# Performance work log

Hardware: AMD Instinct MI355X
Metric: run time of the kernel (lower is better)

The kernel has to match this reference:

```python
import jax, jax.numpy as jnp
import numpy as np


def setup_inputs() -> dict:
    key = jax.random.key(0)
    ks = jax.random.split(key, 7)
    B, T, I, H, O = 128, 1024, 300, 128, 64
    s_ih = 1.0 / np.sqrt(H)
    return {
        "x": jax.random.normal(ks[0], (B, T, I), dtype=jnp.float32),
        "W_ih": jax.random.normal(ks[1], (4 * H, I), dtype=jnp.float32) * s_ih,
        "W_hh": jax.random.normal(ks[2], (4 * H, H), dtype=jnp.float32) * s_ih,
        "b_ih": jax.random.normal(ks[3], (4 * H,), dtype=jnp.float32) * s_ih,
        "b_hh": jax.random.normal(ks[4], (4 * H,), dtype=jnp.float32) * s_ih,
        "W1": jax.random.normal(ks[5], (O, H), dtype=jnp.float32) * s_ih,
        "b1": jax.random.normal(ks[6], (O,), dtype=jnp.float32) * s_ih,
    }


def reference(x, W_ih, W_hh, b_ih, b_hh, W1, b1):
    B, T, I = x.shape
    H = W_hh.shape[1]
    # Precompute the input-to-gate projections for all timesteps at once: [B,T,4H]
    x_gates = jnp.einsum("bti,gi->btg", x, W_ih) + b_ih + b_hh

    def step(carry, xg_t):
        h, c = carry
        gates = xg_t + h @ W_hh.T  # [B, 4H]
        i_g, f_g, g_g, o_g = jnp.split(gates, 4, axis=-1)
        i_g = jax.nn.sigmoid(i_g)
        f_g = jax.nn.sigmoid(f_g)
        g_g = jnp.tanh(g_g)
        o_g = jax.nn.sigmoid(o_g)
        c_new = f_g * c + i_g * g_g
        h_new = o_g * jnp.tanh(c_new)
        return (h_new, c_new), h_new

    h0 = jnp.zeros((B, H), dtype=x.dtype)
    c0 = jnp.zeros((B, H), dtype=x.dtype)
    _, all_h = jax.lax.scan(step, (h0, c0), jnp.swapaxes(x_gates, 0, 1))  # [T,B,H]
    h_seq = jnp.swapaxes(all_h, 0, 1)  # [B,T,H]
    # Dropout in eval mode (identity) for a deterministic reference.
    y = jnp.einsum("bth,oh->bto", h_seq, W1) + b1
    return y
```

## Files before the change

### kernel.cpp

```cpp
#include <hip/hip_runtime.h>
#include <hip/hip_fp16.h>

typedef __attribute__((ext_vector_type(8))) short  s16x8;
typedef __attribute__((ext_vector_type(4))) float  f32x4;
typedef __attribute__((ext_vector_type(4))) unsigned short u16x4;
typedef _Float16 f16x2 __attribute__((ext_vector_type(2)));
typedef _Float16 f16x8 __attribute__((ext_vector_type(8)));
typedef unsigned short u16;

#define MFMA16B(A, B, C) __builtin_amdgcn_mfma_f32_16x16x32_bf16((A), (B), (C), 0, 0, 0)
#define MFMA16H(A, B, C) __builtin_amdgcn_mfma_f32_16x16x32_f16((A), (B), (C), 0, 0, 0)

static __device__ __forceinline__ u16 f2bf(float f) {
    union { float f; unsigned u; } v; v.f = f;
    unsigned r = (v.u + 0x7fffu + ((v.u >> 16) & 1u)) >> 16;
    return (u16)r;
}

static __device__ __forceinline__ s16x8 pack_f16x8(float4 a, float4 b) {
    s16x8 r;
    r[0] = (short)__half_as_ushort(__float2half_rn(a.x));
    r[1] = (short)__half_as_ushort(__float2half_rn(a.y));
    r[2] = (short)__half_as_ushort(__float2half_rn(a.z));
    r[3] = (short)__half_as_ushort(__float2half_rn(a.w));
    r[4] = (short)__half_as_ushort(__float2half_rn(b.x));
    r[5] = (short)__half_as_ushort(__float2half_rn(b.y));
    r[6] = (short)__half_as_ushort(__float2half_rn(b.z));
    r[7] = (short)__half_as_ushort(__float2half_rn(b.w));
    return r;
}

static __device__ __forceinline__ unsigned pk2f16(float a, float b) {
    unsigned lo = __half_as_ushort(__float2half_rn(a));
    unsigned hi = __half_as_ushort(__float2half_rn(b));
    return lo | (hi << 16);
}

static __device__ __forceinline__ float hu2f(u16 v) {
    __half_raw hr; hr.x = v; return __half2float(__half(hr));
}

static __device__ __forceinline__ float dot2(unsigned a, unsigned b, float c) {
#if __has_builtin(__builtin_amdgcn_fdot2)
    return __builtin_amdgcn_fdot2(__builtin_bit_cast(f16x2, a),
                                  __builtin_bit_cast(f16x2, b), c, false);
#else
    f16x2 av = __builtin_bit_cast(f16x2, a), bv = __builtin_bit_cast(f16x2, b);
    return fmaf((float)av[0], (float)bv[0], fmaf((float)av[1], (float)bv[1], c));
#endif
}

static __device__ __forceinline__ float sigm(float x) {
    return __builtin_amdgcn_rcpf(1.f + __expf(-x));
}
static __device__ __forceinline__ float tanh_f(float x) {
    float e = __expf(-2.f * x);
    return fmaf(2.f, __builtin_amdgcn_rcpf(1.f + e), -1.f);
}

static __device__ __forceinline__ void wg_barrier() {
    asm volatile("s_waitcnt lgkmcnt(0)\n\ts_barrier" ::: "memory");
}

#define DPPB(v, ctrl) __builtin_bit_cast(float, __builtin_amdgcn_update_dpp(    \
        0, __builtin_bit_cast(int, (v)), (ctrl), 0xf, 0xf, true))

__global__ __launch_bounds__(256, 2)
void k1_gemm_xgates(const float* __restrict__ x, const float* __restrict__ W_ih,
                    const float* __restrict__ b_ih, const float* __restrict__ b_hh,
                    __half* __restrict__ xg) {
    const int n0 = blockIdx.x * 128;
    const int m0 = blockIdx.y * 128;
    const int tid = threadIdx.x;
    const int wave = tid >> 6, lane = tid & 63;
    const int lanelo = lane & 15, quad = lane >> 4;
    const int mw = (wave & 1) * 64, nw = (wave >> 1) * 64;

    __shared__ __align__(16) u16 As[128 * 40];
    __shared__ __align__(16) u16 Bs[128 * 40];

    f32x4 acc[4][4];
#pragma unroll
    for (int i = 0; i < 4; ++i)
#pragma unroll
        for (int j = 0; j < 4; ++j) acc[i][j] = (f32x4)0.f;

    const int srow = tid >> 1;
    const int scol = (tid & 1) * 16;
    const int grow = (srow & 3) * 128 + (n0 >> 2) + (srow >> 2);

    for (int kc = 0; kc < 10; ++kc) {
        const int k0 = kc * 32;
        const float* srcA = x + (size_t)(m0 + srow) * 300 + k0 + scol;
        const float* srcB = W_ih + (size_t)grow * 300 + k0 + scol;
        if (kc < 9) {
#pragma unroll
            for (int i = 0; i < 4; ++i) {
                const int col = scol + i * 4;
                float4 v = *(const float4*)(srcA + i * 4);
                u16x4 w; w.x = f2bf(v.x); w.y = f2bf(v.y); w.z = f2bf(v.z); w.w = f2bf(v.w);
                *(u16x4*)&As[srow * 40 + col] = w;
                float4 u = *(const float4*)(srcB + i * 4);
                u16x4 q; q.x = f2bf(u.x); q.y = f2bf(u.y); q.z = f2bf(u.z); q.w = f2bf(u.w);
                *(u16x4*)&Bs[srow * 40 + col] = q;
            }
        } else {
#pragma unroll
            for (int i = 0; i < 4; ++i) {
                const int col = scol + i * 4;
                float4 v = {0.f, 0.f, 0.f, 0.f}, u = {0.f, 0.f, 0.f, 0.f};
                if (k0 + col + 3 < 300) { v = *(const float4*)(srcA + i * 4);
                                          u = *(const float4*)(srcB + i * 4); }
                u16x4 w; w.x = f2bf(v.x); w.y = f2bf(v.y); w.z = f2bf(v.z); w.w = f2bf(v.w);
                *(u16x4*)&As[srow * 40 + col] = w;
                u16x4 q; q.x = f2bf(u.x); q.y = f2bf(u.y); q.z = f2bf(u.z); q.w = f2bf(u.w);
                *(u16x4*)&Bs[srow * 40 + col] = q;
            }
        }
        __syncthreads();

        s16x8 af[4], bf[4];
#pragma unroll
        for (int mt = 0; mt < 4; ++mt)
            af[mt] = *(const s16x8*)&As[(mw + mt * 16 + lanelo) * 40 + quad * 8];
#pragma unroll
        for (int nt = 0; nt < 4; ++nt)
            bf[nt] = *(const s16x8*)&Bs[(nw + nt * 16 + lanelo) * 40 + quad * 8];
#pragma unroll
        for (int mt = 0; mt < 4; ++mt)
#pragma unroll
            for (int nt = 0; nt < 4; ++nt)
                acc[mt][nt] = MFMA16B(af[mt], bf[nt], acc[mt][nt]);
        __syncthreads();
    }

#pragma unroll
    for (int nt = 0; nt < 4; ++nt) {
        const int n = n0 + nw + nt * 16 + lanelo;
        const int g = (n & 3) * 128 + (n >> 2);
        const float bs = b_ih[g] + b_hh[g];
#pragma unroll
        for (int mt = 0; mt < 4; ++mt) {
            const int mr = m0 + mw + mt * 16 + quad * 4;
#pragma unroll
            for (int r = 0; r < 4; ++r)
                xg[(size_t)(mr + r) * 512 + n] = __float2half(acc[mt][nt][r] + bs);
        }
    }
}

__global__ __launch_bounds__(512, 2)
void k2_lstm_rec(const __half* __restrict__ xg_all, const float* __restrict__ W_hh,
                 __half* __restrict__ h_seq) {
    const int b = blockIdx.x;
    const int tid = threadIdx.x;
    const int col = tid >> 2;
    const int g = tid & 3;

    __shared__ __align__(16) unsigned hbuf[2][64];

    unsigned wr[64];
    {
        const float2* rp = (const float2*)(W_hh + (size_t)(g * 128 + col) * 128);
#pragma unroll
        for (int k = 0; k < 64; ++k) { float2 a = rp[k]; wr[k] = pk2f16(a.x, a.y); }
    }

    const float sb = (g == 2) ? 2.f : 1.f;
    const float bb = (g == 2) ? -1.f : 0.f;

    const u16* xp = (const u16*)xg_all + (size_t)b * 1024 * 512 + tid;
    u16 xa = xp[0];
    u16 xb = xp[512];

    if (tid < 64) hbuf[0][tid] = 0u;
    float c = 0.f;
    __half* hout = h_seq + (size_t)b * 1024 * 128 + col;
    __syncthreads();

#define STEP(T, RB, WB, XR, NXT) do {                                           \
        const uint4* _hp = (const uint4*)&hbuf[RB][0];                          \
        float _s0 = 0.f, _s1 = 0.f, _s2 = 0.f, _s3 = 0.f;                       \
        _Pragma("unroll")                                                       \
        for (int _j = 0; _j < 16; ++_j) {                                       \
            const uint4 _hv = _hp[_j];                                          \
            const int _k = _j * 4;                                              \
            _s0 = dot2(wr[_k + 0], _hv.x, _s0);                                 \
            _s1 = dot2(wr[_k + 1], _hv.y, _s1);                                 \
            _s2 = dot2(wr[_k + 2], _hv.z, _s2);                                 \
            _s3 = dot2(wr[_k + 3], _hv.w, _s3);                                 \
        }                                                                       \
        const float _pre = (_s0 + _s1) + (_s2 + _s3) + hu2f(XR);                \
        XR = xp[(size_t)(NXT) * 512];                     \
        const float _act = fmaf(sb, sigm(sb * _pre), bb);                       \
        const float _ig = DPPB(_act, 0x00);                    \
        const float _fg = DPPB(_act, 0x55);                    \
        const float _gg = DPPB(_act, 0xAA);                    \
        const float _og = DPPB(_act, 0xFF);                    \
        c = fmaf(_fg, c, _ig * _gg);                                            \
        const float _hv_ = _og * tanh_f(c);                                     \
        const __half _hh = __float2half(_hv_);                                  \
        if (g == 0) ((u16*)&hbuf[WB][0])[col] = (u16)__half_as_ushort(_hh);     \
        if (g == 1) hout[(size_t)(T) * 128] = _hh;         \
        wg_barrier();                                         \
    } while (0)

    for (int t = 0; t < 1024; t += 2) {
        STEP(t,     0, 1, xa, (t + 2 < 1024 ? t + 2 : 1023));
        STEP(t + 1, 1, 0, xb, (t + 3 < 1024 ? t + 3 : 1023));
    }
#undef STEP
}

__global__ __launch_bounds__(256, 2)
void k3_gemm_out(const u16* __restrict__ hseq, const float* __restrict__ W1,
                 const float* __restrict__ b1, float* __restrict__ y) {
    const int m0 = blockIdx.x * 128;
    const int tid = threadIdx.x;
    const int wave = tid >> 6, lane = tid & 63;
    const int lanelo = lane & 15, quad = lane >> 4;

    __shared__ __align__(16) u16 Ah[128 * 136];
    __shared__ __align__(16) u16 Bw[64 * 136];
    __shared__ float b1s[64];

    {
        const int row = tid >> 1, cg = (tid & 1) * 64;
        const u16* src = hseq + (size_t)(m0 + row) * 128 + cg;
#pragma unroll
        for (int i = 0; i < 8; ++i)
            *(s16x8*)&Ah[row * 136 + cg + i * 8] = *(const s16x8*)(src + i * 8);
    }
    {
        const int row = tid >> 2, cg = (tid & 3) * 32;
        const float* src = W1 + (size_t)row * 128 + cg;
#pragma unroll
        for (int i = 0; i < 4; ++i) {
            float4 v0 = *(const float4*)(src + i * 8);
            float4 v1 = *(const float4*)(src + i * 8 + 4);
            *(s16x8*)&Bw[row * 136 + cg + i * 8] = pack_f16x8(v0, v1);
        }
    }
    if (tid < 64) b1s[tid] = b1[tid];
    __syncthreads();

    f16x8 af[2][4], bf[4][4];
#pragma unroll
    for (int mt = 0; mt < 2; ++mt)
#pragma unroll
        for (int kt = 0; kt < 4; ++kt)
            af[mt][kt] = __builtin_bit_cast(f16x8,
                *(const s16x8*)&Ah[(wave * 32 + mt * 16 + lanelo) * 136 + kt * 32 + quad * 8]);
#pragma unroll
    for (int nt = 0; nt < 4; ++nt)
#pragma unroll
        for (int kt = 0; kt < 4; ++kt)
            bf[nt][kt] = __builtin_bit_cast(f16x8,
                *(const s16x8*)&Bw[(nt * 16 + lanelo) * 136 + kt * 32 + quad * 8]);

    f32x4 acc[2][4];
#pragma unroll
    for (int mt = 0; mt < 2; ++mt)
#pragma unroll
        for (int nt = 0; nt < 4; ++nt) acc[mt][nt] = (f32x4)0.f;
#pragma unroll
    for (int kt = 0; kt < 4; ++kt)
#pragma unroll
        for (int mt = 0; mt < 2; ++mt)
#pragma unroll
            for (int nt = 0; nt < 4; ++nt)
                acc[mt][nt] = MFMA16H(af[mt][kt], bf[nt][kt], acc[mt][nt]);

#pragma unroll
    for (int mt = 0; mt < 2; ++mt)
#pragma unroll
        for (int nt = 0; nt < 4; ++nt) {
            const int n = nt * 16 + lanelo;
            const float bs = b1s[n];
            const int mr = m0 + wave * 32 + mt * 16 + quad * 4;
#pragma unroll
            for (int r = 0; r < 4; ++r)
                y[(size_t)(mr + r) * 64 + n] = acc[mt][nt][r] + bs;
        }
}

extern "C" void kernel_launch(void* const* d_in, const int* in_sizes, int n_in,
                              void* d_out, int out_size, void* d_ws, size_t ws_size,
                              hipStream_t stream) {
    const float* x    = (const float*)d_in[0];
    const float* W_ih = (const float*)d_in[1];
    const float* W_hh = (const float*)d_in[2];
    const float* b_ih = (const float*)d_in[3];
    const float* b_hh = (const float*)d_in[4];
    const float* W1   = (const float*)d_in[5];
    const float* b1   = (const float*)d_in[6];
    float* y = (float*)d_out;

    const size_t XG_BYTES = (size_t)131072 * 512 * 2;
    const size_t HS_BYTES = (size_t)131072 * 128 * 2;
    if (ws_size < XG_BYTES + HS_BYTES) return;

    __half* xg   = (__half*)d_ws;
    __half* hseq = (__half*)((char*)d_ws + XG_BYTES);

    k1_gemm_xgates<<<dim3(4, 1024), 256, 0, stream>>>(x, W_ih, b_ih, b_hh, xg);
    k2_lstm_rec<<<128, 512, 0, stream>>>(xg, W_hh, hseq);
    k3_gemm_out<<<1024, 256, 0, stream>>>((const u16*)hseq, W1, b1, y);
}
```

Measured before the change: 909.1 us.

## Compute LSTM recurrent matvec with f16 MFMA instead of per-thread dot2 loops

The recurrent h@W_hh product is moved from 64 fdot2 operations per thread onto 16x16x32 f16 MFMA instructions. W_hh is held as B fragments in registers, and only row 0 of the A tile carries h; the other rows read a zero block. Results pass through LDS so each lane receives its gate preactivation. This cuts VALU work on the serial critical path, but adds MFMA latency, an LDS round trip and wasted rows in every step.

```diff
diff --git a/kernel.cpp b/kernel.cpp
--- a/kernel.cpp
+++ b/kernel.cpp
@@ -30,24 +30,8 @@
     return r;
 }
 
-static __device__ __forceinline__ unsigned pk2f16(float a, float b) {
-    unsigned lo = __half_as_ushort(__float2half_rn(a));
-    unsigned hi = __half_as_ushort(__float2half_rn(b));
-    return lo | (hi << 16);
-}
-
 static __device__ __forceinline__ float hu2f(u16 v) {
     __half_raw hr; hr.x = v; return __half2float(__half(hr));
-}
-
-static __device__ __forceinline__ float dot2(unsigned a, unsigned b, float c) {
-#if __has_builtin(__builtin_amdgcn_fdot2)
-    return __builtin_amdgcn_fdot2(__builtin_bit_cast(f16x2, a),
-                                  __builtin_bit_cast(f16x2, b), c, false);
-#else
-    f16x2 av = __builtin_bit_cast(f16x2, a), bv = __builtin_bit_cast(f16x2, b);
-    return fmaf((float)av[0], (float)bv[0], fmaf((float)av[1], (float)bv[1], c));
-#endif
 }
 
 static __device__ __forceinline__ float sigm(float x) {
@@ -60,6 +44,10 @@
 
 static __device__ __forceinline__ void wg_barrier() {
     asm volatile("s_waitcnt lgkmcnt(0)\n\ts_barrier" ::: "memory");
+}
+
+static __device__ __forceinline__ void lds_fence() {
+    asm volatile("s_waitcnt lgkmcnt(0)" ::: "memory");
 }
 
 #define DPPB(v, ctrl) __builtin_bit_cast(float, __builtin_amdgcn_update_dpp(    \
@@ -154,17 +142,28 @@
                  __half* __restrict__ h_seq) {
     const int b = blockIdx.x;
     const int tid = threadIdx.x;
-    const int col = tid >> 2;
-    const int g = tid & 3;
-
-    __shared__ __align__(16) unsigned hbuf[2][64];
-
-    unsigned wr[64];
-    {
-        const float2* rp = (const float2*)(W_hh + (size_t)(g * 128 + col) * 128);
-#pragma unroll
-        for (int k = 0; k < 64; ++k) { float2 a = rp[k]; wr[k] = pk2f16(a.x, a.y); }
-    }
+    const int w = tid >> 6;
+    const int l = tid & 63;
+    const int col = 16 * w + (l >> 2);
+    const int g = l & 3;
+    const bool row0 = (l & 15) == 0;
+
+    __shared__ __align__(16) u16  hbuf[2][128];
+    __shared__ __align__(16) u16  zblk[104];
+    __shared__ __align__(16) float gate_lds[512];
+
+    f16x8 bfrag[4][4];
+#pragma unroll
+    for (int t = 0; t < 4; ++t)
+#pragma unroll
+        for (int ks = 0; ks < 4; ++ks) {
+            const int n = 64 * w + 16 * t + (l & 15);
+            const int grow = (n & 3) * 128 + (n >> 2);
+            const float* p = W_hh + (size_t)grow * 128 + 32 * ks + (l >> 4) * 8;
+            float4 v0 = *(const float4*)p;
+            float4 v1 = *(const float4*)(p + 4);
+            bfrag[t][ks] = __builtin_bit_cast(f16x8, pack_f16x8(v0, v1));
+        }
 
     const float sb = (g == 2) ? 2.f : 1.f;
     const float bb = (g == 2) ? -1.f : 0.f;
@@ -173,24 +172,54 @@
     u16 xa = xp[0];
     u16 xb = xp[512];
 
-    if (tid < 64) hbuf[0][tid] = 0u;
+    if (tid < 128) hbuf[0][tid] = 0;
+    if (tid < 104) zblk[tid] = 0;
+
+    const u16* aA0 = row0 ? &hbuf[0][(l >> 4) * 8] : &zblk[0];
+    const u16* aA1 = row0 ? &hbuf[1][(l >> 4) * 8] : &zblk[0];
+    float* gw = &gate_lds[64 * w + l];
+    const float* gr = &gate_lds[64 * w + l];
+
     float c = 0.f;
     __half* hout = h_seq + (size_t)b * 1024 * 128 + col;
     __syncthreads();
 
-#define STEP(T, RB, WB, XR, NXT) do {                                           \
-        const uint4* _hp = (const uint4*)&hbuf[RB][0];                          \
-        float _s0 = 0.f, _s1 = 0.f, _s2 = 0.f, _s3 = 0.f;                       \
-        _Pragma("unroll")                                                       \
-        for (int _j = 0; _j < 16; ++_j) {                                       \
-            const uint4 _hv = _hp[_j];                                          \
-            const int _k = _j * 4;                                              \
-            _s0 = dot2(wr[_k + 0], _hv.x, _s0);                                 \
-            _s1 = dot2(wr[_k + 1], _hv.y, _s1);                                 \
-            _s2 = dot2(wr[_k + 2], _hv.z, _s2);                                 \
-            _s3 = dot2(wr[_k + 3], _hv.w, _s3);                                 \
+#define STEP(T, APTR, WB, XR, NXT) do {                                         \
+        s16x8 _a0 = *(const s16x8*)(APTR);                                      \
+        s16x8 _a1 = *(const s16x8*)(APTR + 32);                                 \
+        s16x8 _a2 = *(const s16x8*)(APTR + 64);                                 \
+        s16x8 _a3 = *(const s16x8*)(APTR + 96);                                 \
+        f32x4 _ac0 = (f32x4)0.f, _ac1 = (f32x4)0.f;                             \
+        f32x4 _ac2 = (f32x4)0.f, _ac3 = (f32x4)0.f;                             \
+        f16x8 _af;                                                              \
+        _af = __builtin_bit_cast(f16x8, _a0);                                   \
+        _ac0 = MFMA16H(_af, bfrag[0][0], _ac0);                                 \
+        _ac1 = MFMA16H(_af, bfrag[1][0], _ac1);                                 \
+        _ac2 = MFMA16H(_af, bfrag[2][0], _ac2);                                 \
+        _ac3 = MFMA16H(_af, bfrag[3][0], _ac3);                                 \
+        _af = __builtin_bit_cast(f16x8, _a1);                                   \
+        _ac0 = MFMA16H(_af, bfrag[0][1], _ac0);                                 \
+        _ac1 = MFMA16H(_af, bfrag[1][1], _ac1);                                 \
+        _ac2 = MFMA16H(_af, bfrag[2][1], _ac2);                                 \
+        _ac3 = MFMA16H(_af, bfrag[3][1], _ac3);                                 \
+        _af = __builtin_bit_cast(f16x8, _a2);                                   \
+        _ac0 = MFMA16H(_af, bfrag[0][2], _ac0);                                 \
+        _ac1 = MFMA16H(_af, bfrag[1][2], _ac1);                                 \
+        _ac2 = MFMA16H(_af, bfrag[2][2], _ac2);                                 \
+        _ac3 = MFMA16H(_af, bfrag[3][2], _ac3);                                 \
+        _af = __builtin_bit_cast(f16x8, _a3);                                   \
+        _ac0 = MFMA16H(_af, bfrag[0][3], _ac0);                                 \
+        _ac1 = MFMA16H(_af, bfrag[1][3], _ac1);                                 \
+        _ac2 = MFMA16H(_af, bfrag[2][3], _ac2);                                 \
+        _ac3 = MFMA16H(_af, bfrag[3][3], _ac3);                                 \
+        if (l < 16) {           \
+            gw[0]  = _ac0[0];                                                   \
+            gw[16] = _ac1[0];                                                   \
+            gw[32] = _ac2[0];                                                   \
+            gw[48] = _ac3[0];                                                   \
         }                                                                       \
-        const float _pre = (_s0 + _s1) + (_s2 + _s3) + hu2f(XR);                \
+        lds_fence();                        \
+        const float _pre = *gr + hu2f(XR);                                      \
         XR = xp[(size_t)(NXT) * 512];                     \
         const float _act = fmaf(sb, sigm(sb * _pre), bb);                       \
         const float _ig = DPPB(_act, 0x00);                    \
@@ -198,16 +227,16 @@
         const float _gg = DPPB(_act, 0xAA);                    \
         const float _og = DPPB(_act, 0xFF);                    \
         c = fmaf(_fg, c, _ig * _gg);                                            \
-        const float _hv_ = _og * tanh_f(c);                                     \
-        const __half _hh = __float2half(_hv_);                                  \
-        if (g == 0) ((u16*)&hbuf[WB][0])[col] = (u16)__half_as_ushort(_hh);     \
+        const float _hv = _og * tanh_f(c);                                      \
+        const __half _hh = __float2half(_hv);                                   \
+        if (g == 0) hbuf[WB][col] = (u16)__half_as_ushort(_hh);                 \
         if (g == 1) hout[(size_t)(T) * 128] = _hh;         \
         wg_barrier();                                         \
     } while (0)
 
     for (int t = 0; t < 1024; t += 2) {
-        STEP(t,     0, 1, xa, (t + 2 < 1024 ? t + 2 : 1023));
-        STEP(t + 1, 1, 0, xb, (t + 3 < 1024 ? t + 3 : 1023));
+        STEP(t,     aA0, 1, xa, (t + 2 < 1024 ? t + 2 : 1023));
+        STEP(t + 1, aA1, 0, xb, (t + 3 < 1024 ? t + 3 : 1023));
     }
 #undef STEP
 }
```

Measured after the change: 884.9 us. 1.03x faster.
